# Performance work log

Measured on AMD Instinct MI355X. Metric: run time of the kernel, lower is better.

The kernel has to match this reference:

```python
import jax, jax.numpy as jnp
import numpy as np

N_USERS, N_MOVIES = 200000, 80000
E, L = 2000000, 500000
D, H = 128, 64


def _mean_agg(x_src, src, dst, n_dst):
    # gather source features along edges and mean-reduce per destination node
    msg = x_src[src]                                        # [E, F]
    s = jax.ops.segment_sum(msg, dst, num_segments=n_dst)   # [n_dst, F]
    c = jax.ops.segment_sum(jnp.ones(src.shape, x_src.dtype), dst, num_segments=n_dst)
    return s / jnp.maximum(c, 1.0)[:, None]


def _sage(x_src, x_dst, src, dst, n_dst, Wl, b, Wr):
    # PyG SAGEConv (mean aggr): lin_l(mean_j x_j) + lin_r(x_dst); lin_r has no bias
    return _mean_agg(x_src, src, dst, n_dst) @ Wl + b + x_dst @ Wr


def setup_inputs() -> dict:
    key = jax.random.key(0)
    ks = jax.random.split(key, 24)
    inp = {
        "x_user": jax.random.normal(ks[0], (N_USERS, D), jnp.float32),
        "x_movie": jax.random.normal(ks[1], (N_MOVIES, D), jnp.float32),
        "edge_src": jax.random.randint(ks[2], (E,), 0, N_USERS, jnp.int32),
        "edge_dst": jax.random.randint(ks[3], (E,), 0, N_MOVIES, jnp.int32),
        "lbl_src": jax.random.randint(ks[4], (L,), 0, N_USERS, jnp.int32),
        "lbl_dst": jax.random.randint(ks[5], (L,), 0, N_MOVIES, jnp.int32),
    }
    def w(k, shape):
        fan_in = shape[0]
        return jax.random.uniform(k, shape, jnp.float32, -1.0, 1.0) / np.sqrt(fan_in)
    # layer 1 (src_dim D -> H), one SAGEConv per relation
    inp["W1_u2m_l"] = w(ks[6], (D, H)); inp["b1_u2m"] = jnp.zeros((H,), jnp.float32)
    inp["W1_u2m_r"] = w(ks[7], (D, H))
    inp["W1_m2u_l"] = w(ks[8], (D, H)); inp["b1_m2u"] = jnp.zeros((H,), jnp.float32)
    inp["W1_m2u_r"] = w(ks[9], (D, H))
    # layer 2 (H -> H)
    inp["W2_u2m_l"] = w(ks[10], (H, H)); inp["b2_u2m"] = jnp.zeros((H,), jnp.float32)
    inp["W2_u2m_r"] = w(ks[11], (H, H))
    inp["W2_m2u_l"] = w(ks[12], (H, H)); inp["b2_m2u"] = jnp.zeros((H,), jnp.float32)
    inp["W2_m2u_r"] = w(ks[13], (H, H))
    # edge decoder MLP
    inp["Wd1"] = w(ks[14], (2 * H, H)); inp["bd1"] = jnp.zeros((H,), jnp.float32)
    inp["Wd2"] = w(ks[15], (H, 1)); inp["bd2"] = jnp.zeros((1,), jnp.float32)
    return inp


def reference(x_user, x_movie, edge_src, edge_dst, lbl_src, lbl_dst,
              W1_u2m_l, b1_u2m, W1_u2m_r, W1_m2u_l, b1_m2u, W1_m2u_r,
              W2_u2m_l, b2_u2m, W2_u2m_r, W2_m2u_l, b2_m2u, W2_m2u_r,
              Wd1, bd1, Wd2, bd2):
    # hetero layer 1 (user->movie and movie->user reverse relation), then ReLU
    h_m = jax.nn.relu(_sage(x_user, x_movie, edge_src, edge_dst, N_MOVIES,
                            W1_u2m_l, b1_u2m, W1_u2m_r))
    h_u = jax.nn.relu(_sage(x_movie, x_user, edge_dst, edge_src, N_USERS,
                            W1_m2u_l, b1_m2u, W1_m2u_r))
    # hetero layer 2 (no activation, matching GNNEncoder)
    z_m = _sage(h_u, h_m, edge_src, edge_dst, N_MOVIES, W2_u2m_l, b2_u2m, W2_u2m_r)
    z_u = _sage(h_m, h_u, edge_dst, edge_src, N_USERS, W2_m2u_l, b2_m2u, W2_m2u_r)
    # edge decoder: gather-concat-MLP
    z = jnp.concatenate([z_u[lbl_src], z_m[lbl_dst]], axis=-1)  # [L, 2H]
    z = jax.nn.relu(z @ Wd1 + bd1)
    return (z @ Wd2 + bd2).reshape(-1)
```

## Files before the change

kernel.cpp:

```cpp
#include <hip/hip_runtime.h>
#include <stdint.h>

#define BW   128
#define NBM  625
#define NBU  1563
#define CAPM 4096
#define CAPU 2048

typedef __attribute__((ext_vector_type(8))) short bf16x8;
typedef __attribute__((ext_vector_type(4))) float f32x4;

__device__ __forceinline__ float b2f(ushort u) {
    return __uint_as_float((uint32_t)u << 16);
}
__device__ __forceinline__ ushort f2b(float f) {
    uint32_t x = __float_as_uint(f);
    return (ushort)((x + 0x7FFFu + ((x >> 16) & 1u)) >> 16);
}
__device__ __forceinline__ float lo16f(uint32_t v) { return __uint_as_float(v << 16); }
__device__ __forceinline__ float hi16f(uint32_t v) { return __uint_as_float(v & 0xFFFF0000u); }
__device__ __forceinline__ uint32_t packbf2(float x, float y) {
    return (uint32_t)f2b(x) | ((uint32_t)f2b(y) << 16);
}

__global__ __launch_bounds__(256) void bin_kernel(
    const int* __restrict__ src, const int* __restrict__ dst, int E,
    int* __restrict__ gcm, int* __restrict__ gcu,
    uint32_t* __restrict__ Bm, uint32_t* __restrict__ Bu)
{
    __shared__ int hm[NBM], hu[NBU];
    const int CH = 8192;
    int e0 = blockIdx.x * CH;
    int e1 = min(e0 + CH, E);
    int tid = threadIdx.x;
    for (int b = tid; b < NBM; b += 256) hm[b] = 0;
    for (int b = tid; b < NBU; b += 256) hu[b] = 0;
    __syncthreads();
    for (int i = e0 + tid; i < e1; i += 256) {
        atomicAdd(&hm[dst[i] >> 7], 1);
        atomicAdd(&hu[src[i] >> 7], 1);
    }
    __syncthreads();
    for (int b = tid; b < NBM; b += 256) { int c = hm[b]; hm[b] = c ? atomicAdd(&gcm[b], c) : 0; }
    for (int b = tid; b < NBU; b += 256) { int c = hu[b]; hu[b] = c ? atomicAdd(&gcu[b], c) : 0; }
    __syncthreads();
    for (int i = e0 + tid; i < e1; i += 256) {
        int d = dst[i], s = src[i];
        int bm = d >> 7, bu = s >> 7;
        int pm = atomicAdd(&hm[bm], 1);
        if (pm < CAPM) Bm[(size_t)bm * CAPM + pm] = ((uint32_t)(d & 127) << 24) | (uint32_t)s;
        int pu = atomicAdd(&hu[bu], 1);
        if (pu < CAPU) Bu[(size_t)bu * CAPU + pu] = ((uint32_t)(s & 127) << 24) | (uint32_t)d;
    }
}

__global__ __launch_bounds__(256) void sort_bucket2(
    uint32_t* __restrict__ Bm, const int* __restrict__ gcm, int* __restrict__ loffm,
    uint32_t* __restrict__ Bu, const int* __restrict__ gcu, int* __restrict__ loffu)
{
    __shared__ uint32_t rec[CAPM];
    __shared__ uint32_t srt[CAPM];
    __shared__ int hist[BW];
    __shared__ int hoff[BW + 1];
    __shared__ int cur[BW];
    int bid = blockIdx.x, tid = threadIdx.x;
    uint32_t* B; const int* gc; int* loff; int cap; int b;
    if (bid < NBM) { B = Bm; gc = gcm; loff = loffm; cap = CAPM; b = bid; }
    else           { B = Bu; gc = gcu; loff = loffu; cap = CAPU; b = bid - NBM; }
    int cnt = min(gc[b], cap);
    uint32_t* bp = B + (size_t)b * cap;
    for (int i = tid; i < cnt; i += 256) rec[i] = bp[i];
    if (tid < BW) hist[tid] = 0;
    __syncthreads();
    for (int i = tid; i < cnt; i += 256) atomicAdd(&hist[rec[i] >> 24], 1);
    __syncthreads();
    if (tid == 0) {
        int s = 0;
        for (int i = 0; i < BW; ++i) { hoff[i] = s; s += hist[i]; }
        hoff[BW] = s;
    }
    __syncthreads();
    if (tid < BW) cur[tid] = hoff[tid];
    __syncthreads();
    for (int i = tid; i < cnt; i += 256) {
        uint32_t r = rec[i];
        int pos = atomicAdd(&cur[r >> 24], 1);
        srt[pos] = (r & 0xFFFFFFu) << 5;
    }
    __syncthreads();
    for (int i = tid; i < cnt; i += 256) bp[i] = srt[i];
    for (int i = tid; i <= BW; i += 256) loff[(size_t)b * (BW + 1) + i] = hoff[i];
}

__global__ __launch_bounds__(256) void wprep(
    const float* __restrict__ W2ml, const float* __restrict__ W2mr,
    const float* __restrict__ W2ul, const float* __restrict__ W2ur,
    const float* __restrict__ Wd1, const float* __restrict__ bd1,
    const float* __restrict__ b2m, const float* __restrict__ b2u,
    const float* __restrict__ W1ul, const float* __restrict__ W1mr,
    const float* __restrict__ W1ml, const float* __restrict__ W1ur,
    ushort* __restrict__ Wt2_m, ushort* __restrict__ Wt2_u,
    ushort* __restrict__ Wt_u, ushort* __restrict__ Wt_m,
    float* __restrict__ cu, float* __restrict__ cm)
{
    __shared__ float As[4096], Bs[4096];
    int bid = blockIdx.x, tid = threadIdx.x;
    if (bid < 4) {
        const float* A; int brow0; const float* bvec; const float* addb;
        ushort* WtOut; int cofs; float* outc;
        if (bid == 0)      { A = W2ml; brow0 = 0;  bvec = b2m; addb = bd1;    WtOut = Wt2_m; cofs = 0;  outc = cu; }
        else if (bid == 1) { A = W2mr; brow0 = 0;  bvec = 0;   addb = 0;      WtOut = Wt2_u; cofs = 0;  outc = 0;  }
        else if (bid == 2) { A = W2ul; brow0 = 64; bvec = b2u; addb = 0;      WtOut = Wt2_u; cofs = 64; outc = cm; }
        else               { A = W2ur; brow0 = 64; bvec = 0;   addb = 0;      WtOut = Wt2_m; cofs = 64; outc = 0;  }
        for (int i = tid; i < 4096; i += 256) {
            As[i] = A[i];
            Bs[i] = Wd1[(size_t)(brow0 + (i >> 6)) * 64 + (i & 63)];
        }
        __syncthreads();
        int r = tid >> 2, c0 = (tid & 3) * 16;
        float acc[16] = {};
        for (int k = 0; k < 64; ++k) {
            float a = As[r * 64 + k];
            const float* bp = &Bs[k * 64 + c0];
#pragma unroll
            for (int j = 0; j < 16; ++j) acc[j] += a * bp[j];
        }
#pragma unroll
        for (int j = 0; j < 16; ++j)
            WtOut[(size_t)(cofs + c0 + j) * 64 + r] = f2b(acc[j]);
        if (outc && tid < 64) {
            float s = addb ? addb[tid] : 0.f;
            for (int k = 0; k < 64; ++k) s += bvec[k] * Bs[k * 64 + tid];
            outc[tid] = s;
        }
    } else {
        int t = bid - 4;
        const float *Wa, *Wb; ushort* Wt;
        if (t < 64) { Wa = W1ul; Wb = W1mr; Wt = Wt_u; }
        else        { Wa = W1ml; Wb = W1ur; Wt = Wt_m; t -= 64; }
        int idx = t * 256 + tid;
        int c = idx >> 7, k = idx & 127;
        Wt[idx] = f2b((c < 64 ? Wa : Wb)[(size_t)k * 64 + (c & 63)]);
    }
}

template<int RELU>
__global__ __launch_bounds__(256) void agg_csr(
    const uint32_t* __restrict__ Ba, const int* __restrict__ loffa, int capa,
    const uint32_t* __restrict__ ta, const uint32_t* __restrict__ sa,
    const float* __restrict__ biasa, uint32_t* __restrict__ oa, int na, int GA,
    const uint32_t* __restrict__ Bb, const int* __restrict__ loffb, int capb,
    const uint32_t* __restrict__ tb, const uint32_t* __restrict__ sb,
    const float* __restrict__ biasb, uint32_t* __restrict__ ob, int nb)
{
    int bid = blockIdx.x;
    const uint32_t* B; const int* loff; int cap;
    const uint32_t* table; const uint32_t* self; const float* bias;
    uint32_t* out; int n_nodes; int lb;
    if (bid < GA) { B = Ba; loff = loffa; cap = capa; table = ta; self = sa; bias = biasa; out = oa; n_nodes = na; lb = bid; }
    else          { B = Bb; loff = loffb; cap = capb; table = tb; self = sb; bias = biasb; out = ob; n_nodes = nb; lb = bid - GA; }
    int node = lb * 4 + (threadIdx.x >> 6);
    if (node >= n_nodes) return;
    int lane = threadIdx.x & 63;
    int eq = lane >> 4;
    int fq = lane & 15;
    int b = node >> 7, l = node & 127;
    const int* lo = loff + (size_t)b * (BW + 1);
    int beg = lo[l], end = lo[l + 1];
    const uint32_t* bp = B + (size_t)b * cap;
    float a0 = 0.f, a1 = 0.f, a2 = 0.f, a3 = 0.f;
    int p = beg;
    for (; p + 32 <= end; p += 32) {
        uint32_t r0 = bp[p + eq];
        uint32_t r1 = bp[p + 4 + eq];
        uint32_t r2 = bp[p + 8 + eq];
        uint32_t r3 = bp[p + 12 + eq];
        uint32_t r4 = bp[p + 16 + eq];
        uint32_t r5 = bp[p + 20 + eq];
        uint32_t r6 = bp[p + 24 + eq];
        uint32_t r7 = bp[p + 28 + eq];
        uint2 v0 = *(const uint2*)&table[r0 + fq * 2];
        uint2 v1 = *(const uint2*)&table[r1 + fq * 2];
        uint2 v2 = *(const uint2*)&table[r2 + fq * 2];
        uint2 v3 = *(const uint2*)&table[r3 + fq * 2];
        uint2 v4 = *(const uint2*)&table[r4 + fq * 2];
        uint2 v5 = *(const uint2*)&table[r5 + fq * 2];
        uint2 v6 = *(const uint2*)&table[r6 + fq * 2];
        uint2 v7 = *(const uint2*)&table[r7 + fq * 2];
        a0 += lo16f(v0.x) + lo16f(v1.x) + lo16f(v2.x) + lo16f(v3.x)
            + lo16f(v4.x) + lo16f(v5.x) + lo16f(v6.x) + lo16f(v7.x);
        a1 += hi16f(v0.x) + hi16f(v1.x) + hi16f(v2.x) + hi16f(v3.x)
            + hi16f(v4.x) + hi16f(v5.x) + hi16f(v6.x) + hi16f(v7.x);
        a2 += lo16f(v0.y) + lo16f(v1.y) + lo16f(v2.y) + lo16f(v3.y)
            + lo16f(v4.y) + lo16f(v5.y) + lo16f(v6.y) + lo16f(v7.y);
        a3 += hi16f(v0.y) + hi16f(v1.y) + hi16f(v2.y) + hi16f(v3.y)
            + hi16f(v4.y) + hi16f(v5.y) + hi16f(v6.y) + hi16f(v7.y);
    }
    for (; p + 8 <= end; p += 8) {
        uint32_t r0 = bp[p + eq];
        uint32_t r1 = bp[p + 4 + eq];
        uint2 v0 = *(const uint2*)&table[r0 + fq * 2];
        uint2 v1 = *(const uint2*)&table[r1 + fq * 2];
        a0 += lo16f(v0.x) + lo16f(v1.x);
        a1 += hi16f(v0.x) + hi16f(v1.x);
        a2 += lo16f(v0.y) + lo16f(v1.y);
        a3 += hi16f(v0.y) + hi16f(v1.y);
    }
    if (p + 4 <= end) {
        uint32_t r = bp[p + eq];
        uint2 v = *(const uint2*)&table[r + fq * 2];
        a0 += lo16f(v.x); a1 += hi16f(v.x); a2 += lo16f(v.y); a3 += hi16f(v.y);
        p += 4;
    }
    if (eq < end - p) {
        uint32_t r = bp[p + eq];
        uint2 v = *(const uint2*)&table[r + fq * 2];
        a0 += lo16f(v.x); a1 += hi16f(v.x); a2 += lo16f(v.y); a3 += hi16f(v.y);
    }
    a0 += __shfl_xor(a0, 16, 64); a0 += __shfl_xor(a0, 32, 64);
    a1 += __shfl_xor(a1, 16, 64); a1 += __shfl_xor(a1, 32, 64);
    a2 += __shfl_xor(a2, 16, 64); a2 += __shfl_xor(a2, 32, 64);
    a3 += __shfl_xor(a3, 16, 64); a3 += __shfl_xor(a3, 32, 64);
    if (lane < 16) {
        int deg = end - beg;
        float inv = 1.f / (float)(deg > 0 ? deg : 1);
        uint2 sv = *(const uint2*)&self[(size_t)node * 32 + fq * 2];
        float4 bv = *(const float4*)&bias[fq * 4];
        float v0 = a0 * inv + bv.x + lo16f(sv.x);
        float v1 = a1 * inv + bv.y + hi16f(sv.x);
        float v2 = a2 * inv + bv.z + lo16f(sv.y);
        float v3 = a3 * inv + bv.w + hi16f(sv.y);
        if (RELU) {
            v0 = fmaxf(v0, 0.f); v1 = fmaxf(v1, 0.f);
            v2 = fmaxf(v2, 0.f); v3 = fmaxf(v3, 0.f);
        }
        *(uint2*)&out[(size_t)node * 32 + fq * 2] = make_uint2(packbf2(v0, v1), packbf2(v2, v3));
    }
}

__global__ __launch_bounds__(256) void gemm1_mfma(
    const float* __restrict__ Xu, const ushort* __restrict__ Wtu,
    ushort* __restrict__ Ua, ushort* __restrict__ Ub, int Mu, int GU,
    const float* __restrict__ Xm, const ushort* __restrict__ Wtm,
    ushort* __restrict__ Ma, ushort* __restrict__ Mb, int Mm)
{
    constexpr int K = 128;
    int bid = blockIdx.x;
    const float* X; const ushort* Wt; ushort *Ya, *Yb; int row0; int M;
    if (bid < GU) { X = Xu; Wt = Wtu; Ya = Ua; Yb = Ub; row0 = bid * 128; M = Mu; }
    else          { X = Xm; Wt = Wtm; Ya = Ma; Yb = Mb; row0 = (bid - GU) * 128; M = Mm; }
    int tid = threadIdx.x;
    int lane = tid & 63, wr = tid >> 6;
    int r0g = row0 + wr * 32 + (lane & 15);
    int r1g = r0g + 16;
    int kgrp = (lane >> 4) * 8;
    f32x4 acc0[8] = {}, acc1[8] = {};
#pragma unroll
    for (int ks = 0; ks < 4; ++ks) {
        int kb = kgrp + ks * 32;
        float4 z = make_float4(0.f, 0.f, 0.f, 0.f);
        float4 u0 = z, u1 = z, w0 = z, w1 = z;
        if (r0g < M) {
            u0 = *(const float4*)&X[(size_t)r0g * K + kb];
            u1 = *(const float4*)&X[(size_t)r0g * K + kb + 4];
        }
        if (r1g < M) {
            w0 = *(const float4*)&X[(size_t)r1g * K + kb];
            w1 = *(const float4*)&X[(size_t)r1g * K + kb + 4];
        }
        float xs0[8] = {u0.x, u0.y, u0.z, u0.w, u1.x, u1.y, u1.z, u1.w};
        float xs1[8] = {w0.x, w0.y, w0.z, w0.w, w1.x, w1.y, w1.z, w1.w};
        bf16x8 ah0, al0, ah1, al1;
#pragma unroll
        for (int j = 0; j < 8; ++j) {
            ushort h0 = f2b(xs0[j]);
            ah0[j] = (short)h0;
            al0[j] = (short)f2b(xs0[j] - b2f(h0));
            ushort h1 = f2b(xs1[j]);
            ah1[j] = (short)h1;
            al1[j] = (short)f2b(xs1[j] - b2f(h1));
        }
#pragma unroll
        for (int cb = 0; cb < 8; ++cb) {
            bf16x8 b = *(const bf16x8*)&Wt[(size_t)(cb * 16 + (lane & 15)) * K + kb];
            acc0[cb] = __builtin_amdgcn_mfma_f32_16x16x32_bf16(ah0, b, acc0[cb], 0, 0, 0);
            acc0[cb] = __builtin_amdgcn_mfma_f32_16x16x32_bf16(al0, b, acc0[cb], 0, 0, 0);
            acc1[cb] = __builtin_amdgcn_mfma_f32_16x16x32_bf16(ah1, b, acc1[cb], 0, 0, 0);
            acc1[cb] = __builtin_amdgcn_mfma_f32_16x16x32_bf16(al1, b, acc1[cb], 0, 0, 0);
        }
    }
#pragma unroll
    for (int cb = 0; cb < 8; ++cb) {
        ushort* Y = (cb < 4) ? Ya : Yb;
        int cc = (cb * 16 + (lane & 15)) & 63;
#pragma unroll
        for (int reg = 0; reg < 4; ++reg) {
            int g0 = row0 + wr * 32 + (lane >> 4) * 4 + reg;
            if (g0 < M) Y[(size_t)g0 * 64 + cc] = f2b(acc0[cb][reg]);
            int g1 = g0 + 16;
            if (g1 < M) Y[(size_t)g1 * 64 + cc] = f2b(acc1[cb][reg]);
        }
    }
}

__global__ __launch_bounds__(256) void gemm2_mfma(
    const ushort* __restrict__ Xu, const ushort* __restrict__ Wtu,
    ushort* __restrict__ Ua, ushort* __restrict__ Ub, int Mu, int GU,
    const ushort* __restrict__ Xm, const ushort* __restrict__ Wtm,
    ushort* __restrict__ Ma, ushort* __restrict__ Mb, int Mm)
{
    int bid = blockIdx.x;
    const ushort* X; const ushort* Wt; ushort *Ya, *Yb; int row0;
    if (bid < GU) { X = Xu; Wt = Wtu; Ya = Ua; Yb = Ub; row0 = bid * 64; }
    else          { X = Xm; Wt = Wtm; Ya = Ma; Yb = Mb; row0 = (bid - GU) * 64; }
    int tid = threadIdx.x;
    int lane = tid & 63, wr = tid >> 6;
    int rglob = row0 + wr * 16 + (lane & 15);
    int kgrp = (lane >> 4) * 8;
    f32x4 acc[8] = {};
#pragma unroll
    for (int ks = 0; ks < 2; ++ks) {
        bf16x8 a = *(const bf16x8*)&X[(size_t)rglob * 64 + kgrp + ks * 32];
#pragma unroll
        for (int cb = 0; cb < 8; ++cb) {
            bf16x8 b = *(const bf16x8*)&Wt[(size_t)(cb * 16 + (lane & 15)) * 64 + kgrp + ks * 32];
            acc[cb] = __builtin_amdgcn_mfma_f32_16x16x32_bf16(a, b, acc[cb], 0, 0, 0);
        }
    }
#pragma unroll
    for (int cb = 0; cb < 8; ++cb) {
        ushort* Y = (cb < 4) ? Ya : Yb;
        int cc = (cb * 16 + (lane & 15)) & 63;
#pragma unroll
        for (int reg = 0; reg < 4; ++reg) {
            int grow = row0 + wr * 16 + (lane >> 4) * 4 + reg;
            Y[(size_t)grow * 64 + cc] = f2b(acc[cb][reg]);
        }
    }
}

__global__ __launch_bounds__(256) void edge_dec(
    const uint32_t* __restrict__ Au, const uint32_t* __restrict__ Am,
    const int* __restrict__ ls, const int* __restrict__ ld,
    const float* __restrict__ Wd2, const float* __restrict__ bd2,
    float* __restrict__ out, int L)
{
    int e0 = blockIdx.x * 32 + (threadIdx.x >> 4) * 2;
    if (e0 >= L) return;
    int e1 = e0 + 1;
    bool has1 = (e1 < L);
    int fq = threadIdx.x & 15;
    float4 w = *(const float4*)&Wd2[fq * 4];
    uint2 a0 = *(const uint2*)&Au[(size_t)ls[e0] * 32 + fq * 2];
    uint2 m0 = *(const uint2*)&Am[(size_t)ld[e0] * 32 + fq * 2];
    uint2 a1 = make_uint2(0u, 0u), m1 = make_uint2(0u, 0u);
    if (has1) {
        a1 = *(const uint2*)&Au[(size_t)ls[e1] * 32 + fq * 2];
        m1 = *(const uint2*)&Am[(size_t)ld[e1] * 32 + fq * 2];
    }
    float v0 = fmaxf(lo16f(a0.x) + lo16f(m0.x), 0.f) * w.x
             + fmaxf(hi16f(a0.x) + hi16f(m0.x), 0.f) * w.y
             + fmaxf(lo16f(a0.y) + lo16f(m0.y), 0.f) * w.z
             + fmaxf(hi16f(a0.y) + hi16f(m0.y), 0.f) * w.w;
    float v1 = fmaxf(lo16f(a1.x) + lo16f(m1.x), 0.f) * w.x
             + fmaxf(hi16f(a1.x) + hi16f(m1.x), 0.f) * w.y
             + fmaxf(lo16f(a1.y) + lo16f(m1.y), 0.f) * w.z
             + fmaxf(hi16f(a1.y) + hi16f(m1.y), 0.f) * w.w;
#pragma unroll
    for (int msk = 8; msk >= 1; msk >>= 1) {
        v0 += __shfl_xor(v0, msk, 64);
        v1 += __shfl_xor(v1, msk, 64);
    }
    if (fq == 0) {
        float b = bd2[0];
        out[e0] = v0 + b;
        if (has1) out[e1] = v1 + b;
    }
}

extern "C" void kernel_launch(void* const* d_in, const int* in_sizes, int n_in,
                              void* d_out, int out_size, void* d_ws, size_t ws_size,
                              hipStream_t stream)
{
    const float* x_user  = (const float*)d_in[0];
    const float* x_movie = (const float*)d_in[1];
    const int*   esrc    = (const int*)d_in[2];
    const int*   edst    = (const int*)d_in[3];
    const int*   lsrc    = (const int*)d_in[4];
    const int*   ldst    = (const int*)d_in[5];
    const float* W1ul = (const float*)d_in[6];
    const float* b1u  = (const float*)d_in[7];
    const float* W1ur = (const float*)d_in[8];
    const float* W1ml = (const float*)d_in[9];
    const float* b1m  = (const float*)d_in[10];
    const float* W1mr = (const float*)d_in[11];
    const float* W2ul = (const float*)d_in[12];
    const float* b2u  = (const float*)d_in[13];
    const float* W2ur = (const float*)d_in[14];
    const float* W2ml = (const float*)d_in[15];
    const float* b2m  = (const float*)d_in[16];
    const float* W2mr = (const float*)d_in[17];
    const float* Wd1  = (const float*)d_in[18];
    const float* bd1  = (const float*)d_in[19];
    const float* Wd2  = (const float*)d_in[20];
    const float* bd2  = (const float*)d_in[21];
    float* out = (float*)d_out;

    const int NU = in_sizes[0] / 128;
    const int NM = in_sizes[1] / 128;
    const int E  = in_sizes[2];
    const int L  = in_sizes[4];

    char* ws = (char*)d_ws;
    const size_t SU = (size_t)NU * 64 * 2;
    const size_t SM = (size_t)NM * 64 * 2;
    ushort* U0 = (ushort*)(ws + 0);
    ushort* U1 = (ushort*)(ws + SU);
    ushort* U2 = (ushort*)(ws + 2 * SU);
    ushort* M0 = (ushort*)(ws + 3 * SU);
    ushort* M1 = (ushort*)(ws + 3 * SU + SM);
    ushort* M2 = (ushort*)(ws + 3 * SU + 2 * SM);
    size_t o = 3 * SU + 3 * SM;
    auto align256 = [](size_t x) { return (x + 255) & ~(size_t)255; };
    o = align256(o);
    int* gcm = (int*)(ws + o); o = align256(o + (size_t)(NBM + NBU) * 4);
    int* gcu = gcm + NBM;
    uint32_t* Bm = (uint32_t*)(ws + o); o = align256(o + (size_t)NBM * CAPM * 4);
    uint32_t* Bu = (uint32_t*)(ws + o); o = align256(o + (size_t)NBU * CAPU * 4);
    int* loffm = (int*)(ws + o); o = align256(o + (size_t)NBM * (BW + 1) * 4);
    int* loffu = (int*)(ws + o); o = align256(o + (size_t)NBU * (BW + 1) * 4);
    float* cu  = (float*)(ws + o); o = align256(o + 64 * 4);
    float* cm  = (float*)(ws + o); o = align256(o + 64 * 4);
    ushort* Wt_u  = (ushort*)(ws + o); o = align256(o + 128 * 128 * 2);
    ushort* Wt_m  = (ushort*)(ws + o); o = align256(o + 128 * 128 * 2);
    ushort* Wt2_m = (ushort*)(ws + o); o = align256(o + 128 * 64 * 2);
    ushort* Wt2_u = (ushort*)(ws + o); o = align256(o + 128 * 64 * 2);

    hipMemsetAsync(gcm, 0, (size_t)(NBM + NBU) * 4, stream);
    int nbins = (E + 8191) / 8192;
    bin_kernel<<<nbins, 256, 0, stream>>>(esrc, edst, E, gcm, gcu, Bm, Bu);
    sort_bucket2<<<NBM + NBU, 256, 0, stream>>>(Bm, gcm, loffm, Bu, gcu, loffu);

    wprep<<<4 + 128, 256, 0, stream>>>(W2ml, W2mr, W2ul, W2ur, Wd1, bd1, b2m, b2u,
                                       W1ul, W1mr, W1ml, W1ur,
                                       Wt2_m, Wt2_u, Wt_u, Wt_m, cu, cm);

    int g1u = (NU + 127) / 128, g1m = (NM + 127) / 128;
    int gu = NU / 64, gm = NM / 64;
    int agm = (NM + 3) / 4, agu = (NU + 3) / 4;

    gemm1_mfma<<<g1u + g1m, 256, 0, stream>>>(x_user, Wt_u, U0, U1, NU, g1u,
                                              x_movie, Wt_m, M0, M1, NM);

    agg_csr<1><<<agm + agu, 256, 0, stream>>>(
        Bm, loffm, CAPM, (const uint32_t*)U0, (const uint32_t*)M1, b1u, (uint32_t*)M2, NM, agm,
        Bu, loffu, CAPU, (const uint32_t*)M0, (const uint32_t*)U1, b1m, (uint32_t*)U2, NU);

    gemm2_mfma<<<gu + gm, 256, 0, stream>>>(U2, Wt2_u, U0, U1, NU, gu,
                                            M2, Wt2_m, M0, M1, NM);

    agg_csr<0><<<agm + agu, 256, 0, stream>>>(
        Bm, loffm, CAPM, (const uint32_t*)U1, (const uint32_t*)M1, cm, (uint32_t*)M2, NM, agm,
        Bu, loffu, CAPU, (const uint32_t*)M0, (const uint32_t*)U0, cu, (uint32_t*)U2, NU);

    int gl = (L + 31) / 32;
    edge_dec<<<gl, 256, 0, stream>>>((const uint32_t*)U2, (const uint32_t*)M2,
                                     lsrc, ldst, Wd2, bd2, out, L);
}
```

Baseline: 464.8 us.

## Merge edge binning with layer-1 GEMM and fold memset into weight prep

Replaces the hipMemsetAsync of the bucket counters with an extra block in the weight-prep kernel, so that zeroing happens inside the prep launch. The edge-binning kernel and the first-layer MFMA GEMM become one launch with disjoint block ranges, letting the atomic-heavy binning overlap the compute-bound GEMM and removing launches. The aggregation inner loop is unrolled by 16 instead of 32 edges, giving up some memory-level parallelism for lower register pressure and less tail work. The fused kernel reserves the binning kernel's shared memory for every block, GEMM blocks included, which may reduce GEMM occupancy.

```diff
diff --git a/kernel.cpp b/kernel.cpp
--- a/kernel.cpp
+++ b/kernel.cpp
@@ -23,34 +23,154 @@
     return (uint32_t)f2b(x) | ((uint32_t)f2b(y) << 16);
 }
 
-__global__ __launch_bounds__(256) void bin_kernel(
-    const int* __restrict__ src, const int* __restrict__ dst, int E,
+__global__ __launch_bounds__(256) void prep(
+    const float* __restrict__ W2ml, const float* __restrict__ W2mr,
+    const float* __restrict__ W2ul, const float* __restrict__ W2ur,
+    const float* __restrict__ Wd1, const float* __restrict__ bd1,
+    const float* __restrict__ b2m, const float* __restrict__ b2u,
+    const float* __restrict__ W1ul, const float* __restrict__ W1mr,
+    const float* __restrict__ W1ml, const float* __restrict__ W1ur,
+    ushort* __restrict__ Wt2_m, ushort* __restrict__ Wt2_u,
+    ushort* __restrict__ Wt_u, ushort* __restrict__ Wt_m,
+    float* __restrict__ cu, float* __restrict__ cm,
+    int* __restrict__ gc)
+{
+    __shared__ float As[4096], Bs[4096];
+    int bid = blockIdx.x, tid = threadIdx.x;
+    if (bid < 4) {
+        const float* A; int brow0; const float* bvec; const float* addb;
+        ushort* WtOut; int cofs; float* outc;
+        if (bid == 0)      { A = W2ml; brow0 = 0;  bvec = b2m; addb = bd1;    WtOut = Wt2_m; cofs = 0;  outc = cu; }
+        else if (bid == 1) { A = W2mr; brow0 = 0;  bvec = 0;   addb = 0;      WtOut = Wt2_u; cofs = 0;  outc = 0;  }
+        else if (bid == 2) { A = W2ul; brow0 = 64; bvec = b2u; addb = 0;      WtOut = Wt2_u; cofs = 64; outc = cm; }
+        else               { A = W2ur; brow0 = 64; bvec = 0;   addb = 0;      WtOut = Wt2_m; cofs = 64; outc = 0;  }
+        for (int i = tid; i < 4096; i += 256) {
+            As[i] = A[i];
+            Bs[i] = Wd1[(size_t)(brow0 + (i >> 6)) * 64 + (i & 63)];
+        }
+        __syncthreads();
+        int r = tid >> 2, c0 = (tid & 3) * 16;
+        float acc[16] = {};
+        for (int k = 0; k < 64; ++k) {
+            float a = As[r * 64 + k];
+            const float* bp = &Bs[k * 64 + c0];
+#pragma unroll
+            for (int j = 0; j < 16; ++j) acc[j] += a * bp[j];
+        }
+#pragma unroll
+        for (int j = 0; j < 16; ++j)
+            WtOut[(size_t)(cofs + c0 + j) * 64 + r] = f2b(acc[j]);
+        if (outc && tid < 64) {
+            float s = addb ? addb[tid] : 0.f;
+            for (int k = 0; k < 64; ++k) s += bvec[k] * Bs[k * 64 + tid];
+            outc[tid] = s;
+        }
+    } else if (bid < 132) {
+        int t = bid - 4;
+        const float *Wa, *Wb; ushort* Wt;
+        if (t < 64) { Wa = W1ul; Wb = W1mr; Wt = Wt_u; }
+        else        { Wa = W1ml; Wb = W1ur; Wt = Wt_m; t -= 64; }
+        int idx = t * 256 + tid;
+        int c = idx >> 7, k = idx & 127;
+        Wt[idx] = f2b((c < 64 ? Wa : Wb)[(size_t)k * 64 + (c & 63)]);
+    } else {
+        for (int i = tid; i < NBM + NBU; i += 256) gc[i] = 0;
+    }
+}
+
+__global__ __launch_bounds__(256) void bingemm1(
+    const int* __restrict__ src, const int* __restrict__ dst, int E, int nbins,
     int* __restrict__ gcm, int* __restrict__ gcu,
-    uint32_t* __restrict__ Bm, uint32_t* __restrict__ Bu)
-{
-    __shared__ int hm[NBM], hu[NBU];
-    const int CH = 8192;
-    int e0 = blockIdx.x * CH;
-    int e1 = min(e0 + CH, E);
-    int tid = threadIdx.x;
-    for (int b = tid; b < NBM; b += 256) hm[b] = 0;
-    for (int b = tid; b < NBU; b += 256) hu[b] = 0;
-    __syncthreads();
-    for (int i = e0 + tid; i < e1; i += 256) {
-        atomicAdd(&hm[dst[i] >> 7], 1);
-        atomicAdd(&hu[src[i] >> 7], 1);
-    }
-    __syncthreads();
-    for (int b = tid; b < NBM; b += 256) { int c = hm[b]; hm[b] = c ? atomicAdd(&gcm[b], c) : 0; }
-    for (int b = tid; b < NBU; b += 256) { int c = hu[b]; hu[b] = c ? atomicAdd(&gcu[b], c) : 0; }
-    __syncthreads();
-    for (int i = e0 + tid; i < e1; i += 256) {
-        int d = dst[i], s = src[i];
-        int bm = d >> 7, bu = s >> 7;
-        int pm = atomicAdd(&hm[bm], 1);
-        if (pm < CAPM) Bm[(size_t)bm * CAPM + pm] = ((uint32_t)(d & 127) << 24) | (uint32_t)s;
-        int pu = atomicAdd(&hu[bu], 1);
-        if (pu < CAPU) Bu[(size_t)bu * CAPU + pu] = ((uint32_t)(s & 127) << 24) | (uint32_t)d;
+    uint32_t* __restrict__ Bm, uint32_t* __restrict__ Bu,
+    const float* __restrict__ Xu, const ushort* __restrict__ Wtu,
+    ushort* __restrict__ Ua, ushort* __restrict__ Ub, int Mu, int GU,
+    const float* __restrict__ Xm, const ushort* __restrict__ Wtm,
+    ushort* __restrict__ Ma, ushort* __restrict__ Mb, int Mm)
+{
+    __shared__ int smem[NBM + NBU];
+    int bid = blockIdx.x, tid = threadIdx.x;
+    if (bid < nbins) {
+        int* hm = smem;
+        int* hu = smem + NBM;
+        const int CH = 8192;
+        int e0 = bid * CH;
+        int e1 = min(e0 + CH, E);
+        for (int b = tid; b < NBM; b += 256) hm[b] = 0;
+        for (int b = tid; b < NBU; b += 256) hu[b] = 0;
+        __syncthreads();
+        for (int i = e0 + tid; i < e1; i += 256) {
+            atomicAdd(&hm[dst[i] >> 7], 1);
+            atomicAdd(&hu[src[i] >> 7], 1);
+        }
+        __syncthreads();
+        for (int b = tid; b < NBM; b += 256) { int c = hm[b]; hm[b] = c ? atomicAdd(&gcm[b], c) : 0; }
+        for (int b = tid; b < NBU; b += 256) { int c = hu[b]; hu[b] = c ? atomicAdd(&gcu[b], c) : 0; }
+        __syncthreads();
+        for (int i = e0 + tid; i < e1; i += 256) {
+            int d = dst[i], s = src[i];
+            int bm = d >> 7, bu = s >> 7;
+            int pm = atomicAdd(&hm[bm], 1);
+            if (pm < CAPM) Bm[(size_t)bm * CAPM + pm] = ((uint32_t)(d & 127) << 24) | (uint32_t)s;
+            int pu = atomicAdd(&hu[bu], 1);
+            if (pu < CAPU) Bu[(size_t)bu * CAPU + pu] = ((uint32_t)(s & 127) << 24) | (uint32_t)d;
+        }
+        return;
+    }
+    int gbid = bid - nbins;
+    constexpr int K = 128;
+    const float* X; const ushort* Wt; ushort *Ya, *Yb; int row0; int M;
+    if (gbid < GU) { X = Xu; Wt = Wtu; Ya = Ua; Yb = Ub; row0 = gbid * 128; M = Mu; }
+    else           { X = Xm; Wt = Wtm; Ya = Ma; Yb = Mb; row0 = (gbid - GU) * 128; M = Mm; }
+    int lane = tid & 63, wr = tid >> 6;
+    int r0g = row0 + wr * 32 + (lane & 15);
+    int r1g = r0g + 16;
+    int kgrp = (lane >> 4) * 8;
+    f32x4 acc0[8] = {}, acc1[8] = {};
+#pragma unroll
+    for (int ks = 0; ks < 4; ++ks) {
+        int kb = kgrp + ks * 32;
+        float4 z = make_float4(0.f, 0.f, 0.f, 0.f);
+        float4 u0 = z, u1 = z, w0 = z, w1 = z;
+        if (r0g < M) {
+            u0 = *(const float4*)&X[(size_t)r0g * K + kb];
+            u1 = *(const float4*)&X[(size_t)r0g * K + kb + 4];
+        }
+        if (r1g < M) {
+            w0 = *(const float4*)&X[(size_t)r1g * K + kb];
+            w1 = *(const float4*)&X[(size_t)r1g * K + kb + 4];
+        }
+        float xs0[8] = {u0.x, u0.y, u0.z, u0.w, u1.x, u1.y, u1.z, u1.w};
+        float xs1[8] = {w0.x, w0.y, w0.z, w0.w, w1.x, w1.y, w1.z, w1.w};
+        bf16x8 ah0, al0, ah1, al1;
+#pragma unroll
+        for (int j = 0; j < 8; ++j) {
+            ushort h0 = f2b(xs0[j]);
+            ah0[j] = (short)h0;
+            al0[j] = (short)f2b(xs0[j] - b2f(h0));
+            ushort h1 = f2b(xs1[j]);
+            ah1[j] = (short)h1;
+            al1[j] = (short)f2b(xs1[j] - b2f(h1));
+        }
+#pragma unroll
+        for (int cb = 0; cb < 8; ++cb) {
+            bf16x8 b = *(const bf16x8*)&Wt[(size_t)(cb * 16 + (lane & 15)) * K + kb];
+            acc0[cb] = __builtin_amdgcn_mfma_f32_16x16x32_bf16(ah0, b, acc0[cb], 0, 0, 0);
+            acc0[cb] = __builtin_amdgcn_mfma_f32_16x16x32_bf16(al0, b, acc0[cb], 0, 0, 0);
+            acc1[cb] = __builtin_amdgcn_mfma_f32_16x16x32_bf16(ah1, b, acc1[cb], 0, 0, 0);
+            acc1[cb] = __builtin_amdgcn_mfma_f32_16x16x32_bf16(al1, b, acc1[cb], 0, 0, 0);
+        }
+    }
+#pragma unroll
+    for (int cb = 0; cb < 8; ++cb) {
+        ushort* Y = (cb < 4) ? Ya : Yb;
+        int cc = (cb * 16 + (lane & 15)) & 63;
+#pragma unroll
+        for (int reg = 0; reg < 4; ++reg) {
+            int g0 = row0 + wr * 32 + (lane >> 4) * 4 + reg;
+            if (g0 < M) Y[(size_t)g0 * 64 + cc] = f2b(acc0[cb][reg]);
+            int g1 = g0 + 16;
+            if (g1 < M) Y[(size_t)g1 * 64 + cc] = f2b(acc1[cb][reg]);
+        }
     }
 }
 
@@ -92,58 +212,6 @@
     for (int i = tid; i <= BW; i += 256) loff[(size_t)b * (BW + 1) + i] = hoff[i];
 }
 
-__global__ __launch_bounds__(256) void wprep(
-    const float* __restrict__ W2ml, const float* __restrict__ W2mr,
-    const float* __restrict__ W2ul, const float* __restrict__ W2ur,
-    const float* __restrict__ Wd1, const float* __restrict__ bd1,
-    const float* __restrict__ b2m, const float* __restrict__ b2u,
-    const float* __restrict__ W1ul, const float* __restrict__ W1mr,
-    const float* __restrict__ W1ml, const float* __restrict__ W1ur,
-    ushort* __restrict__ Wt2_m, ushort* __restrict__ Wt2_u,
-    ushort* __restrict__ Wt_u, ushort* __restrict__ Wt_m,
-    float* __restrict__ cu, float* __restrict__ cm)
-{
-    __shared__ float As[4096], Bs[4096];
-    int bid = blockIdx.x, tid = threadIdx.x;
-    if (bid < 4) {
-        const float* A; int brow0; const float* bvec; const float* addb;
-        ushort* WtOut; int cofs; float* outc;
-        if (bid == 0)      { A = W2ml; brow0 = 0;  bvec = b2m; addb = bd1;    WtOut = Wt2_m; cofs = 0;  outc = cu; }
-        else if (bid == 1) { A = W2mr; brow0 = 0;  bvec = 0;   addb = 0;      WtOut = Wt2_u; cofs = 0;  outc = 0;  }
-        else if (bid == 2) { A = W2ul; brow0 = 64; bvec = b2u; addb = 0;      WtOut = Wt2_u; cofs = 64; outc = cm; }
-        else               { A = W2ur; brow0 = 64; bvec = 0;   addb = 0;      WtOut = Wt2_m; cofs = 64; outc = 0;  }
-        for (int i = tid; i < 4096; i += 256) {
-            As[i] = A[i];
-            Bs[i] = Wd1[(size_t)(brow0 + (i >> 6)) * 64 + (i & 63)];
-        }
-        __syncthreads();
-        int r = tid >> 2, c0 = (tid & 3) * 16;
-        float acc[16] = {};
-        for (int k = 0; k < 64; ++k) {
-            float a = As[r * 64 + k];
-            const float* bp = &Bs[k * 64 + c0];
-#pragma unroll
-            for (int j = 0; j < 16; ++j) acc[j] += a * bp[j];
-        }
-#pragma unroll
-        for (int j = 0; j < 16; ++j)
-            WtOut[(size_t)(cofs + c0 + j) * 64 + r] = f2b(acc[j]);
-        if (outc && tid < 64) {
-            float s = addb ? addb[tid] : 0.f;
-            for (int k = 0; k < 64; ++k) s += bvec[k] * Bs[k * 64 + tid];
-            outc[tid] = s;
-        }
-    } else {
-        int t = bid - 4;
-        const float *Wa, *Wb; ushort* Wt;
-        if (t < 64) { Wa = W1ul; Wb = W1mr; Wt = Wt_u; }
-        else        { Wa = W1ml; Wb = W1ur; Wt = Wt_m; t -= 64; }
-        int idx = t * 256 + tid;
-        int c = idx >> 7, k = idx & 127;
-        Wt[idx] = f2b((c < 64 ? Wa : Wb)[(size_t)k * 64 + (c & 63)]);
-    }
-}
-
 template<int RELU>
 __global__ __launch_bounds__(256) void agg_csr(
     const uint32_t* __restrict__ Ba, const int* __restrict__ loffa, int capa,
@@ -170,31 +238,19 @@
     const uint32_t* bp = B + (size_t)b * cap;
     float a0 = 0.f, a1 = 0.f, a2 = 0.f, a3 = 0.f;
     int p = beg;
-    for (; p + 32 <= end; p += 32) {
+    for (; p + 16 <= end; p += 16) {
         uint32_t r0 = bp[p + eq];
         uint32_t r1 = bp[p + 4 + eq];
         uint32_t r2 = bp[p + 8 + eq];
         uint32_t r3 = bp[p + 12 + eq];
-        uint32_t r4 = bp[p + 16 + eq];
-        uint32_t r5 = bp[p + 20 + eq];
-        uint32_t r6 = bp[p + 24 + eq];
-        uint32_t r7 = bp[p + 28 + eq];
         uint2 v0 = *(const uint2*)&table[r0 + fq * 2];
         uint2 v1 = *(const uint2*)&table[r1 + fq * 2];
         uint2 v2 = *(const uint2*)&table[r2 + fq * 2];
         uint2 v3 = *(const uint2*)&table[r3 + fq * 2];
-        uint2 v4 = *(const uint2*)&table[r4 + fq * 2];
-        uint2 v5 = *(const uint2*)&table[r5 + fq * 2];
-        uint2 v6 = *(const uint2*)&table[r6 + fq * 2];
-        uint2 v7 = *(const uint2*)&table[r7 + fq * 2];
-        a0 += lo16f(v0.x) + lo16f(v1.x) + lo16f(v2.x) + lo16f(v3.x)
-            + lo16f(v4.x) + lo16f(v5.x) + lo16f(v6.x) + lo16f(v7.x);
-        a1 += hi16f(v0.x) + hi16f(v1.x) + hi16f(v2.x) + hi16f(v3.x)
-            + hi16f(v4.x) + hi16f(v5.x) + hi16f(v6.x) + hi16f(v7.x);
-        a2 += lo16f(v0.y) + lo16f(v1.y) + lo16f(v2.y) + lo16f(v3.y)
-            + lo16f(v4.y) + lo16f(v5.y) + lo16f(v6.y) + lo16f(v7.y);
-        a3 += hi16f(v0.y) + hi16f(v1.y) + hi16f(v2.y) + hi16f(v3.y)
-            + hi16f(v4.y) + hi16f(v5.y) + hi16f(v6.y) + hi16f(v7.y);
+        a0 += lo16f(v0.x) + lo16f(v1.x) + lo16f(v2.x) + lo16f(v3.x);
+        a1 += hi16f(v0.x) + hi16f(v1.x) + hi16f(v2.x) + hi16f(v3.x);
+        a2 += lo16f(v0.y) + lo16f(v1.y) + lo16f(v2.y) + lo16f(v3.y);
+        a3 += hi16f(v0.y) + hi16f(v1.y) + hi16f(v2.y) + hi16f(v3.y);
     }
     for (; p + 8 <= end; p += 8) {
         uint32_t r0 = bp[p + eq];
@@ -235,71 +291,6 @@
             v2 = fmaxf(v2, 0.f); v3 = fmaxf(v3, 0.f);
         }
         *(uint2*)&out[(size_t)node * 32 + fq * 2] = make_uint2(packbf2(v0, v1), packbf2(v2, v3));
-    }
-}
-
-__global__ __launch_bounds__(256) void gemm1_mfma(
-    const float* __restrict__ Xu, const ushort* __restrict__ Wtu,
-    ushort* __restrict__ Ua, ushort* __restrict__ Ub, int Mu, int GU,
-    const float* __restrict__ Xm, const ushort* __restrict__ Wtm,
-    ushort* __restrict__ Ma, ushort* __restrict__ Mb, int Mm)
-{
-    constexpr int K = 128;
-    int bid = blockIdx.x;
-    const float* X; const ushort* Wt; ushort *Ya, *Yb; int row0; int M;
-    if (bid < GU) { X = Xu; Wt = Wtu; Ya = Ua; Yb = Ub; row0 = bid * 128; M = Mu; }
-    else          { X = Xm; Wt = Wtm; Ya = Ma; Yb = Mb; row0 = (bid - GU) * 128; M = Mm; }
-    int tid = threadIdx.x;
-    int lane = tid & 63, wr = tid >> 6;
-    int r0g = row0 + wr * 32 + (lane & 15);
-    int r1g = r0g + 16;
-    int kgrp = (lane >> 4) * 8;
-    f32x4 acc0[8] = {}, acc1[8] = {};
-#pragma unroll
-    for (int ks = 0; ks < 4; ++ks) {
-        int kb = kgrp + ks * 32;
-        float4 z = make_float4(0.f, 0.f, 0.f, 0.f);
-        float4 u0 = z, u1 = z, w0 = z, w1 = z;
-        if (r0g < M) {
-            u0 = *(const float4*)&X[(size_t)r0g * K + kb];
-            u1 = *(const float4*)&X[(size_t)r0g * K + kb + 4];
-        }
-        if (r1g < M) {
-            w0 = *(const float4*)&X[(size_t)r1g * K + kb];
-            w1 = *(const float4*)&X[(size_t)r1g * K + kb + 4];
-        }
-        float xs0[8] = {u0.x, u0.y, u0.z, u0.w, u1.x, u1.y, u1.z, u1.w};
-        float xs1[8] = {w0.x, w0.y, w0.z, w0.w, w1.x, w1.y, w1.z, w1.w};
-        bf16x8 ah0, al0, ah1, al1;
-#pragma unroll
-        for (int j = 0; j < 8; ++j) {
-            ushort h0 = f2b(xs0[j]);
-            ah0[j] = (short)h0;
-            al0[j] = (short)f2b(xs0[j] - b2f(h0));
-            ushort h1 = f2b(xs1[j]);
-            ah1[j] = (short)h1;
-            al1[j] = (short)f2b(xs1[j] - b2f(h1));
-        }
-#pragma unroll
-        for (int cb = 0; cb < 8; ++cb) {
-            bf16x8 b = *(const bf16x8*)&Wt[(size_t)(cb * 16 + (lane & 15)) * K + kb];
-            acc0[cb] = __builtin_amdgcn_mfma_f32_16x16x32_bf16(ah0, b, acc0[cb], 0, 0, 0);
-            acc0[cb] = __builtin_amdgcn_mfma_f32_16x16x32_bf16(al0, b, acc0[cb], 0, 0, 0);
-            acc1[cb] = __builtin_amdgcn_mfma_f32_16x16x32_bf16(ah1, b, acc1[cb], 0, 0, 0);
-            acc1[cb] = __builtin_amdgcn_mfma_f32_16x16x32_bf16(al1, b, acc1[cb], 0, 0, 0);
-        }
-    }
-#pragma unroll
-    for (int cb = 0; cb < 8; ++cb) {
-        ushort* Y = (cb < 4) ? Ya : Yb;
-        int cc = (cb * 16 + (lane & 15)) & 63;
-#pragma unroll
-        for (int reg = 0; reg < 4; ++reg) {
-            int g0 = row0 + wr * 32 + (lane >> 4) * 4 + reg;
-            if (g0 < M) Y[(size_t)g0 * 64 + cc] = f2b(acc0[cb][reg]);
-            int g1 = g0 + 16;
-            if (g1 < M) Y[(size_t)g1 * 64 + cc] = f2b(acc1[cb][reg]);
-        }
     }
 }
 
@@ -436,21 +427,21 @@
     ushort* Wt2_m = (ushort*)(ws + o); o = align256(o + 128 * 64 * 2);
     ushort* Wt2_u = (ushort*)(ws + o); o = align256(o + 128 * 64 * 2);
 
-    hipMemsetAsync(gcm, 0, (size_t)(NBM + NBU) * 4, stream);
-    int nbins = (E + 8191) / 8192;
-    bin_kernel<<<nbins, 256, 0, stream>>>(esrc, edst, E, gcm, gcu, Bm, Bu);
-    sort_bucket2<<<NBM + NBU, 256, 0, stream>>>(Bm, gcm, loffm, Bu, gcu, loffu);
-
-    wprep<<<4 + 128, 256, 0, stream>>>(W2ml, W2mr, W2ul, W2ur, Wd1, bd1, b2m, b2u,
-                                       W1ul, W1mr, W1ml, W1ur,
-                                       Wt2_m, Wt2_u, Wt_u, Wt_m, cu, cm);
-
     int g1u = (NU + 127) / 128, g1m = (NM + 127) / 128;
     int gu = NU / 64, gm = NM / 64;
     int agm = (NM + 3) / 4, agu = (NU + 3) / 4;
-
-    gemm1_mfma<<<g1u + g1m, 256, 0, stream>>>(x_user, Wt_u, U0, U1, NU, g1u,
-                                              x_movie, Wt_m, M0, M1, NM);
+    int nbins = (E + 8191) / 8192;
+
+    prep<<<133, 256, 0, stream>>>(W2ml, W2mr, W2ul, W2ur, Wd1, bd1, b2m, b2u,
+                                  W1ul, W1mr, W1ml, W1ur,
+                                  Wt2_m, Wt2_u, Wt_u, Wt_m, cu, cm, gcm);
+
+    bingemm1<<<nbins + g1u + g1m, 256, 0, stream>>>(
+        esrc, edst, E, nbins, gcm, gcu, Bm, Bu,
+        x_user, Wt_u, U0, U1, NU, g1u,
+        x_movie, Wt_m, M0, M1, NM);
+
+    sort_bucket2<<<NBM + NBU, 256, 0, stream>>>(Bm, gcm, loffm, Bu, gcu, loffu);
 
     agg_csr<1><<<agm + agu, 256, 0, stream>>>(
         Bm, loffm, CAPM, (const uint32_t*)U0, (const uint32_t*)M1, b1u, (uint32_t*)M2, NM, agm,
```

Result: no change. 456.2 us (-1.8%).
